# Optimization experiments

Hardware: AMD Instinct MI355X
Metric: run time of the kernel (lower is better)

## Reference

```python
import jax, jax.numpy as jnp
import numpy as np

MIN_EXPERT_CAPACITY = 4
CAPACITY_FACTOR = 1.0


def setup_inputs() -> dict:
    key = jax.random.key(0)
    k0, k1, k2, k3 = jax.random.split(key, 4)
    B, S, D, E, F = 4, 2048, 1024, 8, 4096
    x = jax.random.normal(k0, (B, S, D), dtype=jnp.float32)
    router_w = jax.random.normal(k1, (D, E), dtype=jnp.float32) * (D ** -0.5)
    w1 = jax.random.normal(k2, (E, D, F), dtype=jnp.float32) * (D ** -0.5)
    b1 = jnp.zeros((E, F), dtype=jnp.float32)
    w2 = jax.random.normal(k3, (E, F, D), dtype=jnp.float32) * (F ** -0.5)
    b2 = jnp.zeros((E, D), dtype=jnp.float32)
    return {"x": x, "router_w": router_w, "w1": w1, "b1": b1, "w2": w2, "b2": b2}


def _moe_forward(x, router_w, w1, b1, w2, b2):
    B, S, D = x.shape
    E = router_w.shape[1]
    G = 1  # num_groups (single device -> all-to-all is identity)
    T = B * S  # tokens per group
    C = max(int(round(CAPACITY_FACTOR * T / E)), MIN_EXPERT_CAPACITY)

    xt = x.reshape(G, T, D)
    # ---- top-1 tokens-choose masked router ----
    logits = jnp.einsum('gtd,de->gte', xt, router_w)
    probs = jax.nn.softmax(logits, axis=-1)
    gate = jnp.max(probs, axis=-1)          # [g, t]
    idx = jnp.argmax(probs, axis=-1)        # [g, t]
    emask = jax.nn.one_hot(idx, E, dtype=x.dtype)  # [g, t, e]
    # position of each token within its chosen expert's buffer (0-based);
    # -1 for unselected slots -> one_hot gives zeros
    pos = jnp.cumsum(emask, axis=1) * emask - 1.0
    pos = pos.astype(jnp.int32)
    # drop tokens beyond capacity
    slot = jax.nn.one_hot(pos, C, dtype=x.dtype)   # [g, t, e, c]
    dispatch = emask[..., None] * slot             # [g, t, e, c] (0/1)
    combine = dispatch * gate[..., None, None]     # [g, t, e, c]

    # ---- dispatch / expert FFN / combine ----
    expert_inputs = jnp.einsum('gtd,gtec->gecd', xt, dispatch)        # [g, e, c, d]
    h = jax.nn.relu(jnp.einsum('gecd,edf->gecf', expert_inputs, w1) + b1[None, :, None, :])
    expert_outputs = jnp.einsum('gecf,efd->gecd', h, w2) + b2[None, :, None, :]
    out = jnp.einsum('gecd,gtec->gtd', expert_outputs, combine)       # [g, t, d]
    return out.reshape(B, S, D)


def reference(x, router_w, w1, b1, w2, b2):
    return _moe_forward(x, router_w, w1, b1, w2, b2)
```

## Files before the change

### kernel.cpp

```cpp
#include <hip/hip_runtime.h>
#include <hip/hip_fp16.h>

typedef unsigned short ushort_t;
typedef __attribute__((ext_vector_type(8))) _Float16 half8v;
typedef __attribute__((ext_vector_type(4))) float float4v;
typedef __attribute__((ext_vector_type(8))) unsigned short ushort8v;

#define DEV_INLINE __device__ __forceinline__

DEV_INLINE ushort_t f2h_bits(float f) {
  return __half_as_ushort(__float2half(f));
}

__global__ __launch_bounds__(256) void router_kernel(
    const float* __restrict__ x, const float* __restrict__ rw,
    int* __restrict__ idx, float* __restrict__ gate)
{
  constexpr int D = 1024, E = 8;
  int token = (int)((blockIdx.x * 256 + threadIdx.x) >> 6);
  int lane = threadIdx.x & 63;
  const float* xr = x + (size_t)token * D;
  float acc[E];
#pragma unroll
  for (int e = 0; e < E; ++e) acc[e] = 0.f;
  for (int d = lane; d < D; d += 64) {
    float xv = xr[d];
#pragma unroll
    for (int e = 0; e < E; ++e) acc[e] += xv * rw[d * E + e];
  }
#pragma unroll
  for (int off = 32; off >= 1; off >>= 1) {
#pragma unroll
    for (int e = 0; e < E; ++e) acc[e] += __shfl_xor(acc[e], off);
  }
  if (lane == 0) {
    float m = acc[0]; int am = 0;
#pragma unroll
    for (int e = 1; e < E; ++e) { if (acc[e] > m) { m = acc[e]; am = e; } }
    float s = 0.f;
#pragma unroll
    for (int e = 0; e < E; ++e) s += __expf(acc[e] - m);
    idx[token] = am;
    gate[token] = 1.0f / s;
  }
}

__global__ __launch_bounds__(1024) void scan_kernel(
    const int* __restrict__ idx, const float* __restrict__ gate,
    int* __restrict__ slotmap, float* __restrict__ gate_slot)
{
  constexpr int C = 1024, E = 8;
  __shared__ unsigned long long s0[1024];
  __shared__ unsigned long long s1[1024];
  int tid = threadIdx.x;
  int myidx[8];
  unsigned long long c0 = 0, c1 = 0;
#pragma unroll
  for (int j = 0; j < 8; ++j) {
    int e = idx[tid * 8 + j];
    myidx[j] = e;
    if (e < 4) c0 += 1ull << (16 * e);
    else       c1 += 1ull << (16 * (e - 4));
  }
  s0[tid] = c0; s1[tid] = c1;
  __syncthreads();
  for (int off = 1; off < 1024; off <<= 1) {
    unsigned long long b0 = 0, b1 = 0;
    if (tid >= off) { b0 = s0[tid - off]; b1 = s1[tid - off]; }
    __syncthreads();
    s0[tid] += b0; s1[tid] += b1;
    __syncthreads();
  }
  unsigned long long p0 = s0[tid] - c0, p1 = s1[tid] - c1;
  unsigned long long t0 = s0[1023], t1 = s1[1023];
  int cnt[E];
#pragma unroll
  for (int e = 0; e < 4; ++e) {
    cnt[e]     = (int)((p0 >> (16 * e)) & 0xFFFF);
    cnt[4 + e] = (int)((p1 >> (16 * e)) & 0xFFFF);
  }
#pragma unroll
  for (int j = 0; j < 8; ++j) {
    int t = tid * 8 + j;
    int e = myidx[j];
    int pos = cnt[e]++;
    if (pos < C) {
      slotmap[e * C + pos] = t;
      gate_slot[e * C + pos] = gate[t];
    }
  }
  int total[E];
#pragma unroll
  for (int e = 0; e < 4; ++e) {
    total[e]     = (int)((t0 >> (16 * e)) & 0xFFFF);
    total[4 + e] = (int)((t1 >> (16 * e)) & 0xFFFF);
  }
  for (int s = tid; s < E * C; s += 1024) {
    int e = s / C, c = s % C;
    if (c >= total[e]) { slotmap[s] = -1; gate_slot[s] = 0.f; }
  }
}

__global__ __launch_bounds__(256) void gather_kernel(
    const float* __restrict__ x, const int* __restrict__ slotmap,
    ushort_t* __restrict__ Xe)
{
  constexpr int D = 1024;
  int slot = blockIdx.x;
  int t = slotmap[slot];
  int tid = threadIdx.x;
  ushort4* dst = (ushort4*)(Xe + (size_t)slot * D);
  ushort4 o;
  if (t >= 0) {
    float4 v = ((const float4*)(x + (size_t)t * D))[tid];
    o.x = f2h_bits(v.x); o.y = f2h_bits(v.y); o.z = f2h_bits(v.z); o.w = f2h_bits(v.w);
  } else {
    o.x = 0; o.y = 0; o.z = 0; o.w = 0;
  }
  dst[tid] = o;
}

__global__ __launch_bounds__(256) void transpose_cvt(
    const float* __restrict__ in, ushort_t* __restrict__ out, int R, int Cc)
{
  __shared__ ushort_t tile[64][65];
  size_t base = (size_t)blockIdx.z * (size_t)R * (size_t)Cc;
  int c0 = blockIdx.x * 64, r0 = blockIdx.y * 64;
  int tx = threadIdx.x & 63, ty = threadIdx.x >> 6;
#pragma unroll
  for (int i = 0; i < 16; ++i) {
    int r = ty + 4 * i;
    tile[r][tx] = f2h_bits(in[base + (size_t)(r0 + r) * Cc + c0 + tx]);
  }
  __syncthreads();
#pragma unroll
  for (int i = 0; i < 2; ++i) {
    int chunk = (int)threadIdx.x + i * 256;
    int c = chunk >> 3, g = chunk & 7;
    ushort8v v;
#pragma unroll
    for (int j = 0; j < 8; ++j) v[j] = tile[8 * g + j][c];
    *(ushort8v*)(out + base + (size_t)(c0 + c) * R + r0 + 8 * g) = v;
  }
}

#define BAR()   asm volatile("s_barrier" ::: "memory")
#define LGKM0() asm volatile("s_waitcnt lgkmcnt(0)" ::: "memory")
#define VM2()   asm volatile("s_waitcnt vmcnt(2)" ::: "memory")
#define VM0()   asm volatile("s_waitcnt vmcnt(0)" ::: "memory")

#define RD_A(buf, mg) do { _Pragma("unroll") for (int i_ = 0; i_ < 4; ++i_) { \
  _Pragma("unroll") for (int kh_ = 0; kh_ < 2; ++kh_) \
    afr[i_][kh_] = *(const half8v*)&lds[buf][kh_*KH + (arow + ((mg)*4+i_)*16)*32 + axor]; } } while(0)

#define RD_B(buf, np) do { _Pragma("unroll") for (int j_ = 0; j_ < 2; ++j_) { \
  _Pragma("unroll") for (int kh_ = 0; kh_ < 2; ++kh_) \
    bfr[(np)*2+j_][kh_] = *(const half8v*)&lds[buf][AELEM + kh_*KH + (brow + ((np)*2+j_)*16)*32 + axor]; } } while(0)

#define MFMA_Q(mg, np) do { __builtin_amdgcn_s_setprio(1); \
  _Pragma("unroll") for (int i_ = 0; i_ < 4; ++i_) { \
  _Pragma("unroll") for (int j_ = 0; j_ < 2; ++j_) { \
    acc[(mg)*4+i_][(np)*2+j_] = __builtin_amdgcn_mfma_f32_16x16x32_f16(afr[i_][0], bfr[(np)*2+j_][0], acc[(mg)*4+i_][(np)*2+j_], 0, 0, 0); \
    acc[(mg)*4+i_][(np)*2+j_] = __builtin_amdgcn_mfma_f32_16x16x32_f16(afr[i_][1], bfr[(np)*2+j_][1], acc[(mg)*4+i_][(np)*2+j_], 0, 0, 0); } } \
  __builtin_amdgcn_s_setprio(0); } while(0)

template<int KFULL, int NTM, int NTN, int SK, int MODE>
__global__ __launch_bounds__(512, 2) void gemm8p(
    const ushort_t* __restrict__ A, const ushort_t* __restrict__ Bt,
    const float* __restrict__ bias,
    ushort_t* __restrict__ Hout, float* __restrict__ outp,
    const int* __restrict__ slotmap, const float* __restrict__ gate_slot)
{
  constexpr int M_ = NTM * 256, N_ = NTN * 256;
  constexpr int KB = KFULL / SK;
  constexpr int NT = KB / 64;
  constexpr int NU = NT / 2;
  constexpr int KH = 256 * 32;
  constexpr int AELEM = 2 * KH;
  constexpr int WPB = NTM * NTN * SK;
  constexpr int NWG = 8 * WPB;
  constexpr int CPX = NWG / 8;

  __shared__ __attribute__((aligned(16))) ushort_t lds[2][2 * AELEM];

  const int bid = blockIdx.x;
  const int swz = (bid & 7) * CPX + (bid >> 3);
  const int e   = swz / WPB;
  int r = swz % WPB;
  const int sk  = r / (NTM * NTN);  r %= NTM * NTN;
  const int nt  = r / NTM;
  const int mt  = r % NTM;
  const int kb0 = sk * KB;

  const ushort_t* Ae = A  + (size_t)e * M_ * KFULL + (size_t)(mt * 256) * KFULL + kb0;
  const ushort_t* Be = Bt + (size_t)e * N_ * KFULL + (size_t)(nt * 256) * KFULL + kb0;

  const int tid  = threadIdx.x;
  const int lane = tid & 63;
  const int w    = tid >> 6;
  const int wr   = w >> 2;
  const int wc   = w & 3;
  const int l15  = lane & 15;
  const int axor = ((lane >> 4) ^ ((l15 >> 1) & 3)) << 3;
  const int arow = wr * 128 + l15;
  const int brow = wc * 64 + l15;

  const int srow = tid >> 2;
  const int su   = tid & 3;
  auto stage = [&](int buf, int isB, int h, int ktile) {
    const ushort_t* base = isB ? Be : Ae;
#pragma unroll
    for (int kh = 0; kh < 2; ++kh) {
      int row = h * 128 + srow;
      int ul  = su ^ ((row >> 1) & 3);
      const ushort_t* src = base + (size_t)row * KFULL + ktile * 64 + kh * 32 + ul * 8;
      __builtin_amdgcn_global_load_lds(
          (const __attribute__((address_space(1))) void*)src,
          (__attribute__((address_space(3))) void*)(&lds[buf][isB * AELEM + kh * KH + h * 4096 + tid * 8]),
          16, 0, 0);
    }
  };

  float4v acc[8][4] = {};
  half8v afr[4][2], bfr[4][2];

  stage(0, 0, 0, 0); stage(0, 0, 1, 0); stage(0, 1, 0, 0); stage(0, 1, 1, 0);
  stage(1, 0, 0, 1);
  VM2(); BAR();

  for (int u = 0; u < NU - 1; ++u) {
    const int t1 = 2 * u + 1, t2 = 2 * u + 2, t3 = 2 * u + 3;
    RD_A(0, 0); RD_B(0, 0); stage(1, 0, 1, t1); BAR(); MFMA_Q(0, 0); BAR();
    RD_B(0, 1);             stage(1, 1, 0, t1); BAR(); MFMA_Q(0, 1); BAR();
    RD_A(0, 1);             stage(1, 1, 1, t1); BAR(); MFMA_Q(1, 0); LGKM0(); BAR();
    stage(0, 0, 0, t2); BAR(); MFMA_Q(1, 1); VM2(); BAR();
    RD_A(1, 0); RD_B(1, 0); stage(0, 0, 1, t2); BAR(); MFMA_Q(0, 0); BAR();
    RD_B(1, 1);             stage(0, 1, 0, t2); BAR(); MFMA_Q(0, 1); BAR();
    RD_A(1, 1);             stage(0, 1, 1, t2); BAR(); MFMA_Q(1, 0); LGKM0(); BAR();
    stage(1, 0, 0, t3); BAR(); MFMA_Q(1, 1); VM2(); BAR();
  }
  {
    const int t1 = NT - 1;
    RD_A(0, 0); RD_B(0, 0); stage(1, 0, 1, t1); BAR(); MFMA_Q(0, 0); BAR();
    RD_B(0, 1);             stage(1, 1, 0, t1); BAR(); MFMA_Q(0, 1); BAR();
    RD_A(0, 1);             stage(1, 1, 1, t1); BAR(); MFMA_Q(1, 0); LGKM0(); BAR();
    MFMA_Q(1, 1); VM0(); BAR();
    RD_A(1, 0); RD_B(1, 0); BAR(); MFMA_Q(0, 0); BAR();
    RD_B(1, 1);             BAR(); MFMA_Q(0, 1); BAR();
    RD_A(1, 1);             BAR(); MFMA_Q(1, 0); BAR();
    MFMA_Q(1, 1);
  }

  const int lr4   = (lane >> 4) * 4;
  const int mbase = mt * 256 + wr * 128;
  const int nbase = nt * 256 + wc * 64;

  float bv[4];
#pragma unroll
  for (int j = 0; j < 4; ++j) bv[j] = bias[e * N_ + nbase + j * 16 + l15];

  if (MODE == 0) {
    ushort_t* He = Hout + (size_t)e * M_ * N_;
#pragma unroll
    for (int i = 0; i < 8; ++i) {
#pragma unroll
      for (int q = 0; q < 4; ++q) {
        int m = mbase + i * 16 + lr4 + q;
#pragma unroll
        for (int j = 0; j < 4; ++j) {
          float v = acc[i][j][q] + bv[j];
          v = v > 0.f ? v : 0.f;
          He[(size_t)m * N_ + nbase + j * 16 + l15] = f2h_bits(v);
        }
      }
    }
  } else {
#pragma unroll
    for (int i = 0; i < 8; ++i) {
#pragma unroll
      for (int q = 0; q < 4; ++q) {
        int slot = e * M_ + mbase + i * 16 + lr4 + q;
        int tkn = slotmap[slot];
        if (tkn < 0) continue;
        float gt = gate_slot[slot];
#pragma unroll
        for (int j = 0; j < 4; ++j) {
          float v = (acc[i][j][q] + (sk == 0 ? bv[j] : 0.f)) * gt;
          atomicAdd(&outp[(size_t)tkn * N_ + nbase + j * 16 + l15], v);
        }
      }
    }
  }
}

extern "C" void kernel_launch(void* const* d_in, const int* in_sizes, int n_in,
                              void* d_out, int out_size, void* d_ws, size_t ws_size,
                              hipStream_t stream)
{
  const float* x  = (const float*)d_in[0];
  const float* rw = (const float*)d_in[1];
  const float* w1 = (const float*)d_in[2];
  const float* b1 = (const float*)d_in[3];
  const float* w2 = (const float*)d_in[4];
  const float* b2 = (const float*)d_in[5];
  float* out = (float*)d_out;

  constexpr int D = 1024, E = 8, F = 4096, T = 8192, C = 1024;

  char* p = (char*)d_ws;
  auto take = [&](size_t bytes) { char* r = p; p += (bytes + 255) & ~(size_t)255; return r; };
  ushort_t* w1t = (ushort_t*)take((size_t)E * D * F * 2);
  ushort_t* w2t = (ushort_t*)take((size_t)E * F * D * 2);
  ushort_t* Xe  = (ushort_t*)take((size_t)E * C * D * 2);
  ushort_t* H   = (ushort_t*)take((size_t)E * C * F * 2);
  int*      idx = (int*)take((size_t)T * 4);
  float*   gate = (float*)take((size_t)T * 4);
  int*  slotmap = (int*)take((size_t)E * C * 4);
  float* gate_slot = (float*)take((size_t)E * C * 4);

  router_kernel<<<T / 4, 256, 0, stream>>>(x, rw, idx, gate);
  scan_kernel<<<1, 1024, 0, stream>>>(idx, gate, slotmap, gate_slot);
  gather_kernel<<<E * C, 256, 0, stream>>>(x, slotmap, Xe);
  transpose_cvt<<<dim3(F / 64, D / 64, E), 256, 0, stream>>>(w1, w1t, D, F);
  transpose_cvt<<<dim3(D / 64, F / 64, E), 256, 0, stream>>>(w2, w2t, F, D);
  hipMemsetAsync(d_out, 0, (size_t)out_size * sizeof(float), stream);
  gemm8p<1024, 4, 16, 1, 0><<<512, 512, 0, stream>>>(
      Xe, w1t, b1, H, nullptr, nullptr, nullptr);
  gemm8p<4096, 4, 4, 2, 1><<<256, 512, 0, stream>>>(
      H, w2t, b2, nullptr, out, slotmap, gate_slot);
}
```

Before: 304.4 us.

## Replace atomic scatter with split-K partial buffers plus combine kernel; rework LDS-read pipeline

The second GEMM now writes plain split-K partial tiles into a reused workspace (the w1t buffer) instead of doing gated atomicAdds into the output. A new combine kernel sums the two partials, adds the bias, scales by the gate and writes each token once, which also removes the output memset. Separately, the GEMM main loop is re-pipelined with separate fragment registers for the two halves of A and B, so LDS reads for the next quadrant are issued ahead of the current MFMAs and some LGKM waits go away. This adds about 64 MB of partial-buffer traffic and one extra launch, and the reworked pipeline uses more registers.

```diff
diff --git a/kernel.cpp b/kernel.cpp
--- a/kernel.cpp
+++ b/kernel.cpp
@@ -46,8 +46,8 @@
 }
 
 __global__ __launch_bounds__(1024) void scan_kernel(
-    const int* __restrict__ idx, const float* __restrict__ gate,
-    int* __restrict__ slotmap, float* __restrict__ gate_slot)
+    const int* __restrict__ idx,
+    int* __restrict__ slotmap, int* __restrict__ tok2slot)
 {
   constexpr int C = 1024, E = 8;
   __shared__ unsigned long long s0[1024];
@@ -86,7 +86,9 @@
     int pos = cnt[e]++;
     if (pos < C) {
       slotmap[e * C + pos] = t;
-      gate_slot[e * C + pos] = gate[t];
+      tok2slot[t] = e * C + pos;
+    } else {
+      tok2slot[t] = -1;
     }
   }
   int total[E];
@@ -97,7 +99,7 @@
   }
   for (int s = tid; s < E * C; s += 1024) {
     int e = s / C, c = s % C;
-    if (c >= total[e]) { slotmap[s] = -1; gate_slot[s] = 0.f; }
+    if (c >= total[e]) slotmap[s] = -1;
   }
 }
 
@@ -144,32 +146,57 @@
   }
 }
 
-#define BAR()   asm volatile("s_barrier" ::: "memory")
-#define LGKM0() asm volatile("s_waitcnt lgkmcnt(0)" ::: "memory")
-#define VM2()   asm volatile("s_waitcnt vmcnt(2)" ::: "memory")
-#define VM0()   asm volatile("s_waitcnt vmcnt(0)" ::: "memory")
-
-#define RD_A(buf, mg) do { _Pragma("unroll") for (int i_ = 0; i_ < 4; ++i_) { \
+__global__ __launch_bounds__(256) void combine_kernel(
+    const float* __restrict__ p, const float* __restrict__ b2,
+    const int* __restrict__ tok2slot, const float* __restrict__ gate,
+    float* __restrict__ out)
+{
+  constexpr int D = 1024;
+  constexpr size_t ECD = (size_t)8 * 1024 * 1024;
+  int t = blockIdx.x;
+  int d4 = threadIdx.x;
+  float4* o = (float4*)(out + (size_t)t * D);
+  int slot = tok2slot[t];
+  if (slot < 0) { o[d4] = make_float4(0.f, 0.f, 0.f, 0.f); return; }
+  int e = slot >> 10;
+  float g = gate[t];
+  float4 a = ((const float4*)(p + (size_t)slot * D))[d4];
+  float4 b = ((const float4*)(p + ECD + (size_t)slot * D))[d4];
+  float4 bb = ((const float4*)(b2 + (size_t)e * D))[d4];
+  o[d4] = make_float4((a.x + b.x + bb.x) * g, (a.y + b.y + bb.y) * g,
+                      (a.z + b.z + bb.z) * g, (a.w + b.w + bb.w) * g);
+}
+
+#define BAR()  asm volatile("s_barrier" ::: "memory")
+#define VM2()  asm volatile("s_waitcnt vmcnt(2)" ::: "memory")
+#define VM4()  asm volatile("s_waitcnt vmcnt(4)" ::: "memory")
+#define VM0()  asm volatile("s_waitcnt vmcnt(0)" ::: "memory")
+
+#define RD_A0(buf) { _Pragma("unroll") for (int i_ = 0; i_ < 4; ++i_) { \
   _Pragma("unroll") for (int kh_ = 0; kh_ < 2; ++kh_) \
-    afr[i_][kh_] = *(const half8v*)&lds[buf][kh_*KH + (arow + ((mg)*4+i_)*16)*32 + axor]; } } while(0)
-
-#define RD_B(buf, np) do { _Pragma("unroll") for (int j_ = 0; j_ < 2; ++j_) { \
+    aS0[i_][kh_] = *(const half8v*)&lds[buf][kh_*KH + (arow + i_*16)*32 + axor]; } }
+#define RD_A1(buf) { _Pragma("unroll") for (int i_ = 0; i_ < 4; ++i_) { \
   _Pragma("unroll") for (int kh_ = 0; kh_ < 2; ++kh_) \
-    bfr[(np)*2+j_][kh_] = *(const half8v*)&lds[buf][AELEM + kh_*KH + (brow + ((np)*2+j_)*16)*32 + axor]; } } while(0)
-
-#define MFMA_Q(mg, np) do { __builtin_amdgcn_s_setprio(1); \
+    aS1[i_][kh_] = *(const half8v*)&lds[buf][kh_*KH + (arow + (4+i_)*16)*32 + axor]; } }
+#define RD_B0(buf) { _Pragma("unroll") for (int j_ = 0; j_ < 2; ++j_) { \
+  _Pragma("unroll") for (int kh_ = 0; kh_ < 2; ++kh_) \
+    bS0[j_][kh_] = *(const half8v*)&lds[buf][AELEM + kh_*KH + (brow + j_*16)*32 + axor]; } }
+#define RD_B1(buf) { _Pragma("unroll") for (int j_ = 0; j_ < 2; ++j_) { \
+  _Pragma("unroll") for (int kh_ = 0; kh_ < 2; ++kh_) \
+    bS1[j_][kh_] = *(const half8v*)&lds[buf][AELEM + kh_*KH + (brow + (2+j_)*16)*32 + axor]; } }
+
+#define MQ(AS, BS, MB, NB) { __builtin_amdgcn_s_setprio(1); \
   _Pragma("unroll") for (int i_ = 0; i_ < 4; ++i_) { \
   _Pragma("unroll") for (int j_ = 0; j_ < 2; ++j_) { \
-    acc[(mg)*4+i_][(np)*2+j_] = __builtin_amdgcn_mfma_f32_16x16x32_f16(afr[i_][0], bfr[(np)*2+j_][0], acc[(mg)*4+i_][(np)*2+j_], 0, 0, 0); \
-    acc[(mg)*4+i_][(np)*2+j_] = __builtin_amdgcn_mfma_f32_16x16x32_f16(afr[i_][1], bfr[(np)*2+j_][1], acc[(mg)*4+i_][(np)*2+j_], 0, 0, 0); } } \
-  __builtin_amdgcn_s_setprio(0); } while(0)
+    acc[(MB)+i_][(NB)+j_] = __builtin_amdgcn_mfma_f32_16x16x32_f16(AS[i_][0], BS[j_][0], acc[(MB)+i_][(NB)+j_], 0, 0, 0); \
+    acc[(MB)+i_][(NB)+j_] = __builtin_amdgcn_mfma_f32_16x16x32_f16(AS[i_][1], BS[j_][1], acc[(MB)+i_][(NB)+j_], 0, 0, 0); } } \
+  __builtin_amdgcn_s_setprio(0); }
 
 template<int KFULL, int NTM, int NTN, int SK, int MODE>
 __global__ __launch_bounds__(512, 2) void gemm8p(
     const ushort_t* __restrict__ A, const ushort_t* __restrict__ Bt,
     const float* __restrict__ bias,
-    ushort_t* __restrict__ Hout, float* __restrict__ outp,
-    const int* __restrict__ slotmap, const float* __restrict__ gate_slot)
+    ushort_t* __restrict__ Hout, float* __restrict__ outp)
 {
   constexpr int M_ = NTM * 256, N_ = NTN * 256;
   constexpr int KB = KFULL / SK;
@@ -222,44 +249,44 @@
   };
 
   float4v acc[8][4] = {};
-  half8v afr[4][2], bfr[4][2];
+  half8v aS0[4][2], aS1[4][2], bS0[2][2], bS1[2][2];
 
   stage(0, 0, 0, 0); stage(0, 0, 1, 0); stage(0, 1, 0, 0); stage(0, 1, 1, 0);
-  stage(1, 0, 0, 1);
-  VM2(); BAR();
+  stage(1, 1, 0, 1); stage(1, 0, 0, 1);
+  VM4(); BAR();
+  RD_A0(0); RD_B0(0);
 
   for (int u = 0; u < NU - 1; ++u) {
     const int t1 = 2 * u + 1, t2 = 2 * u + 2, t3 = 2 * u + 3;
-    RD_A(0, 0); RD_B(0, 0); stage(1, 0, 1, t1); BAR(); MFMA_Q(0, 0); BAR();
-    RD_B(0, 1);             stage(1, 1, 0, t1); BAR(); MFMA_Q(0, 1); BAR();
-    RD_A(0, 1);             stage(1, 1, 1, t1); BAR(); MFMA_Q(1, 0); LGKM0(); BAR();
-    stage(0, 0, 0, t2); BAR(); MFMA_Q(1, 1); VM2(); BAR();
-    RD_A(1, 0); RD_B(1, 0); stage(0, 0, 1, t2); BAR(); MFMA_Q(0, 0); BAR();
-    RD_B(1, 1);             stage(0, 1, 0, t2); BAR(); MFMA_Q(0, 1); BAR();
-    RD_A(1, 1);             stage(0, 1, 1, t2); BAR(); MFMA_Q(1, 0); LGKM0(); BAR();
-    stage(1, 0, 0, t3); BAR(); MFMA_Q(1, 1); VM2(); BAR();
+    RD_B1(0); stage(1, 0, 1, t1); BAR(); MQ(aS0, bS0, 0, 0); BAR();
+    RD_A1(0); stage(1, 1, 1, t1); BAR(); MQ(aS0, bS1, 0, 2); VM2(); BAR();
+    RD_A0(1); stage(0, 1, 0, t2); BAR(); MQ(aS1, bS0, 4, 0); VM2(); BAR();
+    RD_B0(1); stage(0, 0, 0, t2); BAR(); MQ(aS1, bS1, 4, 2); BAR();
+    RD_B1(1); stage(0, 0, 1, t2); BAR(); MQ(aS0, bS0, 0, 0); BAR();
+    RD_A1(1); stage(0, 1, 1, t2); BAR(); MQ(aS0, bS1, 0, 2); VM2(); BAR();
+    RD_A0(0); stage(1, 1, 0, t3); BAR(); MQ(aS1, bS0, 4, 0); VM2(); BAR();
+    RD_B0(0); stage(1, 0, 0, t3); BAR(); MQ(aS1, bS1, 4, 2); BAR();
   }
   {
     const int t1 = NT - 1;
-    RD_A(0, 0); RD_B(0, 0); stage(1, 0, 1, t1); BAR(); MFMA_Q(0, 0); BAR();
-    RD_B(0, 1);             stage(1, 1, 0, t1); BAR(); MFMA_Q(0, 1); BAR();
-    RD_A(0, 1);             stage(1, 1, 1, t1); BAR(); MFMA_Q(1, 0); LGKM0(); BAR();
-    MFMA_Q(1, 1); VM0(); BAR();
-    RD_A(1, 0); RD_B(1, 0); BAR(); MFMA_Q(0, 0); BAR();
-    RD_B(1, 1);             BAR(); MFMA_Q(0, 1); BAR();
-    RD_A(1, 1);             BAR(); MFMA_Q(1, 0); BAR();
-    MFMA_Q(1, 1);
+    RD_B1(0); stage(1, 0, 1, t1); BAR(); MQ(aS0, bS0, 0, 0); BAR();
+    RD_A1(0); stage(1, 1, 1, t1); BAR(); MQ(aS0, bS1, 0, 2); VM2(); BAR();
+    RD_A0(1);                     BAR(); MQ(aS1, bS0, 4, 0); VM0(); BAR();
+    RD_B0(1);                     BAR(); MQ(aS1, bS1, 4, 2); BAR();
+    RD_B1(1);                     BAR(); MQ(aS0, bS0, 0, 0); BAR();
+    RD_A1(1);                     BAR(); MQ(aS0, bS1, 0, 2); BAR();
+                                  BAR(); MQ(aS1, bS0, 4, 0); BAR();
+                                         MQ(aS1, bS1, 4, 2);
   }
 
   const int lr4   = (lane >> 4) * 4;
   const int mbase = mt * 256 + wr * 128;
   const int nbase = nt * 256 + wc * 64;
 
-  float bv[4];
-#pragma unroll
-  for (int j = 0; j < 4; ++j) bv[j] = bias[e * N_ + nbase + j * 16 + l15];
-
   if (MODE == 0) {
+    float bv[4];
+#pragma unroll
+    for (int j = 0; j < 4; ++j) bv[j] = bias[e * N_ + nbase + j * 16 + l15];
     ushort_t* He = Hout + (size_t)e * M_ * N_;
 #pragma unroll
     for (int i = 0; i < 8; ++i) {
@@ -275,18 +302,15 @@
       }
     }
   } else {
+    float* pe = outp + ((size_t)(sk * 8 + e)) * (size_t)M_ * N_;
 #pragma unroll
     for (int i = 0; i < 8; ++i) {
 #pragma unroll
       for (int q = 0; q < 4; ++q) {
-        int slot = e * M_ + mbase + i * 16 + lr4 + q;
-        int tkn = slotmap[slot];
-        if (tkn < 0) continue;
-        float gt = gate_slot[slot];
+        int m = mbase + i * 16 + lr4 + q;
 #pragma unroll
         for (int j = 0; j < 4; ++j) {
-          float v = (acc[i][j][q] + (sk == 0 ? bv[j] : 0.f)) * gt;
-          atomicAdd(&outp[(size_t)tkn * N_ + nbase + j * 16 + l15], v);
+          pe[(size_t)m * N_ + nbase + j * 16 + l15] = acc[i][j][q];
         }
       }
     }
@@ -316,16 +340,16 @@
   int*      idx = (int*)take((size_t)T * 4);
   float*   gate = (float*)take((size_t)T * 4);
   int*  slotmap = (int*)take((size_t)E * C * 4);
-  float* gate_slot = (float*)take((size_t)E * C * 4);
+  int* tok2slot = (int*)take((size_t)T * 4);
+
+  float* partials = (float*)w1t;
 
   router_kernel<<<T / 4, 256, 0, stream>>>(x, rw, idx, gate);
-  scan_kernel<<<1, 1024, 0, stream>>>(idx, gate, slotmap, gate_slot);
+  scan_kernel<<<1, 1024, 0, stream>>>(idx, slotmap, tok2slot);
   gather_kernel<<<E * C, 256, 0, stream>>>(x, slotmap, Xe);
   transpose_cvt<<<dim3(F / 64, D / 64, E), 256, 0, stream>>>(w1, w1t, D, F);
   transpose_cvt<<<dim3(D / 64, F / 64, E), 256, 0, stream>>>(w2, w2t, F, D);
-  hipMemsetAsync(d_out, 0, (size_t)out_size * sizeof(float), stream);
-  gemm8p<1024, 4, 16, 1, 0><<<512, 512, 0, stream>>>(
-      Xe, w1t, b1, H, nullptr, nullptr, nullptr);
-  gemm8p<4096, 4, 4, 2, 1><<<256, 512, 0, stream>>>(
-      H, w2t, b2, nullptr, out, slotmap, gate_slot);
-}
+  gemm8p<1024, 4, 16, 1, 0><<<512, 512, 0, stream>>>(Xe, w1t, b1, H, nullptr);
+  gemm8p<4096, 4, 4, 2, 1><<<256, 512, 0, stream>>>(H, w2t, nullptr, nullptr, partials);
+  combine_kernel<<<T, 256, 0, stream>>>(partials, b2, tok2slot, gate, out);
+}
```

Measured after the change: 284.1 us. 1.07x faster.
